# Kernel tuning notes

Measured on AMD Instinct MI355X. Metric: run time of the kernel, lower is better.

The kernel has to match this reference:

```python
import jax, jax.numpy as jnp
import numpy as np

N, IN_F, OUT_F = 8192, 256, 128
ALPHA = 0.2          # LeakyReLU negative slope
NEG_INF = -9e15      # mask value used by the original module
DENSITY = 0.1        # adjacency density


def setup_inputs() -> dict:
    key = jax.random.key(0)
    k1, k2, k3, k4 = jax.random.split(key, 4)
    x = jax.random.normal(k1, (N, IN_F), dtype=jnp.float32)
    adj = (jax.random.uniform(k2, (N, N)) < DENSITY).astype(jnp.float32)
    W = jax.random.normal(k3, (IN_F, OUT_F), dtype=jnp.float32) * (1.0 / np.sqrt(IN_F))
    a = jax.random.normal(k4, (2 * OUT_F, 1), dtype=jnp.float32) * (1.0 / np.sqrt(2 * OUT_F))
    return {"x": x, "adj": adj, "W": W, "a": a}


def reference(x, adj, W, a):
    # h = x @ W : [N, F]
    h = x @ W
    # Decompose a^T [h_i ; h_j] = (h a1)_i + (h a2)_j  -- identical math to the
    # original O(N^2 * 2F) cat/repeat construction, without materializing it.
    a1 = a[:OUT_F, 0]           # [F]
    a2 = a[OUT_F:, 0]           # [F]
    s1 = h @ a1                 # [N]
    s2 = h @ a2                 # [N]
    e = jax.nn.leaky_relu(s1[:, None] + s2[None, :], negative_slope=ALPHA)  # [N, N]
    scores = jnp.where(adj > 0, e, NEG_INF)
    attention = jax.nn.softmax(scores, axis=1)   # row-wise softmax
    # dropout = 0.0 (eval mode) -> identity
    h_prime = attention @ h      # [N, F]
    return h_prime
```

## Files before the change

### kernel.cpp

```cpp
#include <hip/hip_runtime.h>
#include <hip/hip_bf16.h>

typedef __attribute__((ext_vector_type(4))) float  f32x4;
typedef __attribute__((ext_vector_type(8))) short  bf16x8;
typedef unsigned short u16;

#define ALPHA 0.2f
#define NN 8192
#define FF 128
#define LOG2E 1.4426950408889634f

__device__ __forceinline__ u16 f2b(float f) {
  __hip_bfloat16 hb = __float2bfloat16(f);
  return *reinterpret_cast<u16*>(&hb);
}

extern "C" __global__ void __launch_bounds__(256)
wt_cvt(const float* __restrict__ x, const float* __restrict__ Wm,
       u16* __restrict__ xb, u16* __restrict__ WTb) {
  const int id = blockIdx.x * 256 + threadIdx.x;
  if (blockIdx.x < 2048) {
    const f32x4 v = *(const f32x4*)(x + (size_t)id * 4);
    uint2 p;
    p.x = f2b(v.x) | ((unsigned)f2b(v.y) << 16);
    p.y = f2b(v.z) | ((unsigned)f2b(v.w) << 16);
    *(uint2*)(xb + (size_t)id * 4) = p;
  } else {
    const int o = id - 2048 * 256;
    const int c = o >> 8, k = o & 255;
    WTb[o] = f2b(Wm[k * 128 + c]);
  }
}

extern "C" __global__ void __launch_bounds__(256)
gat_h(const u16* __restrict__ xb, const u16* __restrict__ WTb,
      const float* __restrict__ av, u16* __restrict__ hT2,
      float* __restrict__ s1v, float* __restrict__ s2v) {
  __shared__ float hs[16][128];
  const int t = threadIdx.x, lane = t & 63, wv = t >> 6;
  const int i0 = blockIdx.x * 16;
  const int fr = lane & 15, kg = lane >> 4;

  f32x4 acc0 = {0.f,0.f,0.f,0.f}, acc1 = {0.f,0.f,0.f,0.f};
  const u16* xp  = xb  + (size_t)(i0 + fr) * 256 + kg * 8;
  const u16* b0p = WTb + (size_t)(wv * 32 + fr) * 256 + kg * 8;
  const u16* b1p = b0p + 16 * 256;
#pragma unroll
  for (int ks = 0; ks < 8; ++ks) {
    const bf16x8 A  = *(const bf16x8*)(xp  + ks * 32);
    const bf16x8 B0 = *(const bf16x8*)(b0p + ks * 32);
    const bf16x8 B1 = *(const bf16x8*)(b1p + ks * 32);
    acc0 = __builtin_amdgcn_mfma_f32_16x16x32_bf16(A, B0, acc0, 0, 0, 0);
    acc1 = __builtin_amdgcn_mfma_f32_16x16x32_bf16(A, B1, acc1, 0, 0, 0);
  }
#pragma unroll
  for (int r = 0; r < 4; ++r) {
    hs[kg * 4 + r][wv * 32 + fr]      = acc0[r];
    hs[kg * 4 + r][wv * 32 + 16 + fr] = acc1[r];
  }
  __syncthreads();

  {
    const int c = t >> 1, rr = (t & 1) * 8;
    u16 u[8];
#pragma unroll
    for (int m = 0; m < 8; ++m) u[m] = f2b(hs[rr + m][c]);
    *(uint4*)(hT2 + ((size_t)(i0 >> 5) * 128 + c) * 32 + (i0 & 31) + rr) =
        *(const uint4*)u;
  }
  {
    const int r = t >> 4, q = t & 15;
    float p1 = 0.f, p2 = 0.f;
#pragma unroll
    for (int m = 0; m < 8; ++m) {
      const int c = q * 8 + m;
      const float hv = hs[r][c];
      p1 = fmaf(hv, av[c], p1);
      p2 = fmaf(hv, av[128 + c], p2);
    }
    p1 += __shfl_xor(p1, 1); p1 += __shfl_xor(p1, 2);
    p1 += __shfl_xor(p1, 4); p1 += __shfl_xor(p1, 8);
    p2 += __shfl_xor(p2, 1); p2 += __shfl_xor(p2, 2);
    p2 += __shfl_xor(p2, 4); p2 += __shfl_xor(p2, 8);
    if (q == 0) { s1v[i0 + r] = p1 * LOG2E; s2v[i0 + r] = p2 * LOG2E; }
  }
}

#define MM(BB, AA) AA = __builtin_amdgcn_mfma_f32_16x16x32_bf16(af, BB, AA, 0, 0, 0)

extern "C" __global__ void __launch_bounds__(256, 4)
gat_main(const float* __restrict__ adj, const u16* __restrict__ hT2,
         const float* __restrict__ s1l, const float* __restrict__ s2l,
         float* __restrict__ out) {
  __shared__ float accp[4][16][132];
  __shared__ float denp[4][16];

  const int t = threadIdx.x, lane = t & 63, ks = t >> 6;
  const int fr = lane & 15, kg = lane >> 4;
  const int i0 = blockIdx.x * 16;

  const float s1i = s1l[i0 + fr];
  const float* adjp = adj + (size_t)(i0 + fr) * NN + ks * 32 + kg * 8;
  const float* s2p  = s2l + ks * 32 + kg * 8;
  const u16*   hp   = hT2 + ks * 4096 + fr * 32 + kg * 8;

  f32x4 acc0 = {0,0,0,0}, acc1 = {0,0,0,0}, acc2 = {0,0,0,0}, acc3 = {0,0,0,0};
  f32x4 acc4 = {0,0,0,0}, acc5 = {0,0,0,0}, acc6 = {0,0,0,0}, acc7 = {0,0,0,0};
  float den = 0.f;

  f32x4 a0 = *(const f32x4*)(adjp);
  f32x4 a1 = *(const f32x4*)(adjp + 4);
  f32x4 z0 = *(const f32x4*)(s2p);
  f32x4 z1 = *(const f32x4*)(s2p + 4);

  for (int it = 0; it < 64; ++it) {
    const u16* hb = hp + it * 16384;
    const bf16x8 b0 = *(const bf16x8*)(hb);
    const bf16x8 b1 = *(const bf16x8*)(hb + 512);
    const bf16x8 b2 = *(const bf16x8*)(hb + 1024);
    const bf16x8 b3 = *(const bf16x8*)(hb + 1536);
    const bf16x8 b4 = *(const bf16x8*)(hb + 2048);
    const bf16x8 b5 = *(const bf16x8*)(hb + 2560);
    const bf16x8 b6 = *(const bf16x8*)(hb + 3072);
    const bf16x8 b7 = *(const bf16x8*)(hb + 3584);
    __builtin_amdgcn_sched_barrier(0);

    bf16x8 af;
    float dstep = 0.f;
#pragma unroll
    for (int e = 0; e < 8; ++e) {
      const float adv = (e < 4) ? a0[e] : a1[e - 4];
      const float tz  = s1i + ((e < 4) ? z0[e] : z1[e - 4]);
      const float fz  = fmaxf(tz, ALPHA * tz);
      const float w8  = adv * exp2f(fz);
      dstep += w8;
      af[e] = (short)f2b(w8);
    }
    den += dstep;

    const int itn = it < 63 ? it + 1 : 63;
    const float* an = adjp + itn * 128;
    a0 = *(const f32x4*)(an);
    a1 = *(const f32x4*)(an + 4);
    const float* zn = s2p + itn * 128;
    z0 = *(const f32x4*)(zn);
    z1 = *(const f32x4*)(zn + 4);
    __builtin_amdgcn_sched_barrier(0);

    MM(b0, acc0); MM(b1, acc1); MM(b2, acc2); MM(b3, acc3);
    MM(b4, acc4); MM(b5, acc5); MM(b6, acc6); MM(b7, acc7);
  }

  den += __shfl_xor(den, 16);
  den += __shfl_xor(den, 32);
  if (lane < 16) denp[ks][fr] = den;

#define STACC(F, AA) _Pragma("unroll") \
  for (int r = 0; r < 4; ++r) accp[ks][kg * 4 + r][F * 16 + fr] = AA[r];
  STACC(0, acc0) STACC(1, acc1) STACC(2, acc2) STACC(3, acc3)
  STACC(4, acc4) STACC(5, acc5) STACC(6, acc6) STACC(7, acc7)
#undef STACC

  __syncthreads();

  {
    const int row = t >> 4;
    const int c0  = (t & 15) * 8;
    const float dv = denp[0][row] + denp[1][row] + denp[2][row] + denp[3][row];
    f32x4 sA = {0,0,0,0}, sB = {0,0,0,0};
#pragma unroll
    for (int w = 0; w < 4; ++w) {
      sA += *(const f32x4*)&accp[w][row][c0];
      sB += *(const f32x4*)&accp[w][row][c0 + 4];
    }
    const float inv = 1.f / dv;
    sA *= inv; sB *= inv;
    float* op = out + (size_t)(i0 + row) * FF + c0;
    *(f32x4*)op       = sA;
    *(f32x4*)(op + 4) = sB;
  }
}

extern "C" void kernel_launch(void* const* d_in, const int* in_sizes, int n_in,
                              void* d_out, int out_size, void* d_ws, size_t ws_size,
                              hipStream_t stream) {
  const float* x   = (const float*)d_in[0];
  const float* adj = (const float*)d_in[1];
  const float* Wm  = (const float*)d_in[2];
  const float* av  = (const float*)d_in[3];
  float* out = (float*)d_out;

  char* ws = (char*)d_ws;
  u16*   hT2 = (u16*)(ws);
  float* s1v = (float*)(ws + 2097152);
  float* s2v = (float*)(ws + 2129920);
  u16*   xb  = (u16*)(ws + 2162688);
  u16*   WTb = (u16*)(ws + 6356992);

  wt_cvt  <<<2176, 256, 0, stream>>>(x, Wm, xb, WTb);
  gat_h   <<<NN / 16, 256, 0, stream>>>(xb, WTb, av, hT2, s1v, s2v);
  gat_main<<<NN / 16, 256, 0, stream>>>(adj, hT2, s1v, s2v, out);
}
```

Before: 417.8 us.

## Split columns four ways and compute two row tiles per block with reduction

gat_main now handles 32 rows per block instead of 16, so each h fragment loaded from memory feeds two MFMAs. It also splits the 8192 columns into four quarters across blocks and writes partial numerators and denominators to workspace. A new gat_red kernel sums the four partials and normalises. This aims to halve h-tile traffic and lengthen the MFMA chain per load while keeping 1024 blocks. The cost is more accumulator registers, roughly 16 MB of partial writes and reads, and an extra kernel launch.

```diff
diff --git a/kernel.cpp b/kernel.cpp
--- a/kernel.cpp
+++ b/kernel.cpp
@@ -86,99 +86,153 @@
   }
 }
 
-#define MM(BB, AA) AA = __builtin_amdgcn_mfma_f32_16x16x32_bf16(af, BB, AA, 0, 0, 0)
+#define MM(BB, AA) AA = __builtin_amdgcn_mfma_f32_16x16x32_bf16(af0, BB, AA, 0, 0, 0)
+#define MM1(BB, AA) AA = __builtin_amdgcn_mfma_f32_16x16x32_bf16(af1, BB, AA, 0, 0, 0)
 
 extern "C" __global__ void __launch_bounds__(256, 4)
 gat_main(const float* __restrict__ adj, const u16* __restrict__ hT2,
          const float* __restrict__ s1l, const float* __restrict__ s2l,
-         float* __restrict__ out) {
+         float* __restrict__ nump, float* __restrict__ deng) {
   __shared__ float accp[4][16][132];
   __shared__ float denp[4][16];
 
   const int t = threadIdx.x, lane = t & 63, ks = t >> 6;
   const int fr = lane & 15, kg = lane >> 4;
-  const int i0 = blockIdx.x * 16;
-
-  const float s1i = s1l[i0 + fr];
-  const float* adjp = adj + (size_t)(i0 + fr) * NN + ks * 32 + kg * 8;
-  const float* s2p  = s2l + ks * 32 + kg * 8;
-  const u16*   hp   = hT2 + ks * 4096 + fr * 32 + kg * 8;
-
-  f32x4 acc0 = {0,0,0,0}, acc1 = {0,0,0,0}, acc2 = {0,0,0,0}, acc3 = {0,0,0,0};
-  f32x4 acc4 = {0,0,0,0}, acc5 = {0,0,0,0}, acc6 = {0,0,0,0}, acc7 = {0,0,0,0};
-  float den = 0.f;
-
-  f32x4 a0 = *(const f32x4*)(adjp);
-  f32x4 a1 = *(const f32x4*)(adjp + 4);
+  const int tile = blockIdx.x >> 2, q = blockIdx.x & 3;
+  const int i0 = tile * 32;
+  const int jq = q * 2048;
+
+  const float s1i0 = s1l[i0 + fr];
+  const float s1i1 = s1l[i0 + 16 + fr];
+  const float* adjp0 = adj + (size_t)(i0 + fr) * NN + jq + ks * 32 + kg * 8;
+  const float* adjp1 = adjp0 + (size_t)16 * NN;
+  const float* s2p   = s2l + jq + ks * 32 + kg * 8;
+  const u16*   hp    = hT2 + (size_t)(q * 64 + ks) * 4096 + fr * 32 + kg * 8;
+
+  f32x4 acc0[8], acc1[8];
+#pragma unroll
+  for (int f = 0; f < 8; ++f) { acc0[f] = (f32x4){0,0,0,0}; acc1[f] = (f32x4){0,0,0,0}; }
+  float den0 = 0.f, den1 = 0.f;
+
+  f32x4 a0 = *(const f32x4*)(adjp0);
+  f32x4 a1 = *(const f32x4*)(adjp0 + 4);
+  f32x4 a2 = *(const f32x4*)(adjp1);
+  f32x4 a3 = *(const f32x4*)(adjp1 + 4);
   f32x4 z0 = *(const f32x4*)(s2p);
   f32x4 z1 = *(const f32x4*)(s2p + 4);
 
-  for (int it = 0; it < 64; ++it) {
+  for (int it = 0; it < 16; ++it) {
     const u16* hb = hp + it * 16384;
     const bf16x8 b0 = *(const bf16x8*)(hb);
     const bf16x8 b1 = *(const bf16x8*)(hb + 512);
     const bf16x8 b2 = *(const bf16x8*)(hb + 1024);
     const bf16x8 b3 = *(const bf16x8*)(hb + 1536);
+    __builtin_amdgcn_sched_barrier(0);
+
+    bf16x8 af0, af1;
+    float d0 = 0.f, d1 = 0.f;
+#pragma unroll
+    for (int e = 0; e < 8; ++e) {
+      const float zz  = (e < 4) ? z0[e] : z1[e - 4];
+      const float av0 = (e < 4) ? a0[e] : a1[e - 4];
+      const float av1 = (e < 4) ? a2[e] : a3[e - 4];
+      float t0 = s1i0 + zz; t0 = fmaxf(t0, ALPHA * t0);
+      float t1 = s1i1 + zz; t1 = fmaxf(t1, ALPHA * t1);
+      const float w0 = av0 * exp2f(t0);
+      const float w1 = av1 * exp2f(t1);
+      d0 += w0; d1 += w1;
+      af0[e] = (short)f2b(w0);
+      af1[e] = (short)f2b(w1);
+    }
+    den0 += d0; den1 += d1;
+    __builtin_amdgcn_sched_barrier(0);
+
     const bf16x8 b4 = *(const bf16x8*)(hb + 2048);
     const bf16x8 b5 = *(const bf16x8*)(hb + 2560);
     const bf16x8 b6 = *(const bf16x8*)(hb + 3072);
     const bf16x8 b7 = *(const bf16x8*)(hb + 3584);
     __builtin_amdgcn_sched_barrier(0);
 
-    bf16x8 af;
-    float dstep = 0.f;
-#pragma unroll
-    for (int e = 0; e < 8; ++e) {
-      const float adv = (e < 4) ? a0[e] : a1[e - 4];
-      const float tz  = s1i + ((e < 4) ? z0[e] : z1[e - 4]);
-      const float fz  = fmaxf(tz, ALPHA * tz);
-      const float w8  = adv * exp2f(fz);
-      dstep += w8;
-      af[e] = (short)f2b(w8);
-    }
-    den += dstep;
-
-    const int itn = it < 63 ? it + 1 : 63;
-    const float* an = adjp + itn * 128;
-    a0 = *(const f32x4*)(an);
-    a1 = *(const f32x4*)(an + 4);
-    const float* zn = s2p + itn * 128;
-    z0 = *(const f32x4*)(zn);
-    z1 = *(const f32x4*)(zn + 4);
-    __builtin_amdgcn_sched_barrier(0);
-
-    MM(b0, acc0); MM(b1, acc1); MM(b2, acc2); MM(b3, acc3);
-    MM(b4, acc4); MM(b5, acc5); MM(b6, acc6); MM(b7, acc7);
-  }
-
-  den += __shfl_xor(den, 16);
-  den += __shfl_xor(den, 32);
-  if (lane < 16) denp[ks][fr] = den;
-
-#define STACC(F, AA) _Pragma("unroll") \
-  for (int r = 0; r < 4; ++r) accp[ks][kg * 4 + r][F * 16 + fr] = AA[r];
-  STACC(0, acc0) STACC(1, acc1) STACC(2, acc2) STACC(3, acc3)
-  STACC(4, acc4) STACC(5, acc5) STACC(6, acc6) STACC(7, acc7)
-#undef STACC
-
-  __syncthreads();
-
-  {
-    const int row = t >> 4;
-    const int c0  = (t & 15) * 8;
-    const float dv = denp[0][row] + denp[1][row] + denp[2][row] + denp[3][row];
+    MM(b0, acc0[0]); MM1(b0, acc1[0]); MM(b1, acc0[1]); MM1(b1, acc1[1]);
+    MM(b2, acc0[2]); MM1(b2, acc1[2]); MM(b3, acc0[3]); MM1(b3, acc1[3]);
+
+    const int itn = it < 15 ? it + 1 : 15;
+    a0 = *(const f32x4*)(adjp0 + itn * 128);
+    a1 = *(const f32x4*)(adjp0 + itn * 128 + 4);
+    a2 = *(const f32x4*)(adjp1 + itn * 128);
+    a3 = *(const f32x4*)(adjp1 + itn * 128 + 4);
+    z0 = *(const f32x4*)(s2p + itn * 128);
+    z1 = *(const f32x4*)(s2p + itn * 128 + 4);
+    __builtin_amdgcn_sched_barrier(0);
+
+    MM(b4, acc0[4]); MM1(b4, acc1[4]); MM(b5, acc0[5]); MM1(b5, acc1[5]);
+    MM(b6, acc0[6]); MM1(b6, acc1[6]); MM(b7, acc0[7]); MM1(b7, acc1[7]);
+  }
+
+  const size_t obase = ((size_t)(q * 256 + tile)) * 32;
+
+  {
+    float d = den0;
+    d += __shfl_xor(d, 16); d += __shfl_xor(d, 32);
+    if (lane < 16) denp[ks][fr] = d;
+#pragma unroll
+    for (int f = 0; f < 8; ++f)
+#pragma unroll
+      for (int r = 0; r < 4; ++r) accp[ks][kg * 4 + r][f * 16 + fr] = acc0[f][r];
+    __syncthreads();
+    const int row = t >> 4, c0 = (t & 15) * 8;
     f32x4 sA = {0,0,0,0}, sB = {0,0,0,0};
 #pragma unroll
     for (int w = 0; w < 4; ++w) {
       sA += *(const f32x4*)&accp[w][row][c0];
       sB += *(const f32x4*)&accp[w][row][c0 + 4];
     }
-    const float inv = 1.f / dv;
-    sA *= inv; sB *= inv;
-    float* op = out + (size_t)(i0 + row) * FF + c0;
-    *(f32x4*)op       = sA;
-    *(f32x4*)(op + 4) = sB;
-  }
+    float* op = nump + (obase + row) * FF + c0;
+    *(f32x4*)op = sA; *(f32x4*)(op + 4) = sB;
+    if ((t & 15) == 0)
+      deng[obase + row] = denp[0][row] + denp[1][row] + denp[2][row] + denp[3][row];
+    __syncthreads();
+  }
+  {
+    float d = den1;
+    d += __shfl_xor(d, 16); d += __shfl_xor(d, 32);
+    if (lane < 16) denp[ks][fr] = d;
+#pragma unroll
+    for (int f = 0; f < 8; ++f)
+#pragma unroll
+      for (int r = 0; r < 4; ++r) accp[ks][kg * 4 + r][f * 16 + fr] = acc1[f][r];
+    __syncthreads();
+    const int row = t >> 4, c0 = (t & 15) * 8;
+    f32x4 sA = {0,0,0,0}, sB = {0,0,0,0};
+#pragma unroll
+    for (int w = 0; w < 4; ++w) {
+      sA += *(const f32x4*)&accp[w][row][c0];
+      sB += *(const f32x4*)&accp[w][row][c0 + 4];
+    }
+    float* op = nump + (obase + 16 + row) * FF + c0;
+    *(f32x4*)op = sA; *(f32x4*)(op + 4) = sB;
+    if ((t & 15) == 0)
+      deng[obase + 16 + row] = denp[0][row] + denp[1][row] + denp[2][row] + denp[3][row];
+  }
+}
+
+extern "C" __global__ void __launch_bounds__(256)
+gat_red(const float* __restrict__ nump, const float* __restrict__ deng,
+        float* __restrict__ out) {
+  const int gid = blockIdx.x * 256 + threadIdx.x;
+  const int i = gid >> 5, c4 = (gid & 31) * 4;
+  const int tile = i >> 5, row = i & 31;
+  f32x4 s = {0,0,0,0};
+  float dv = 0.f;
+#pragma unroll
+  for (int q = 0; q < 4; ++q) {
+    const size_t rb = ((size_t)(q * 256 + tile)) * 32 + row;
+    s  += *(const f32x4*)(nump + rb * FF + c4);
+    dv += deng[rb];
+  }
+  const float inv = 1.f / dv;
+  s *= inv;
+  *(f32x4*)(out + (size_t)i * FF + c4) = s;
 }
 
 extern "C" void kernel_launch(void* const* d_in, const int* in_sizes, int n_in,
@@ -196,8 +250,11 @@
   float* s2v = (float*)(ws + 2129920);
   u16*   xb  = (u16*)(ws + 2162688);
   u16*   WTb = (u16*)(ws + 6356992);
+  float* nump = (float*)(ws + 6422528);
+  float* deng = (float*)(ws + 23199744);
 
   wt_cvt  <<<2176, 256, 0, stream>>>(x, Wm, xb, WTb);
   gat_h   <<<NN / 16, 256, 0, stream>>>(xb, WTb, av, hT2, s1v, s2v);
-  gat_main<<<NN / 16, 256, 0, stream>>>(adj, hT2, s1v, s2v, out);
-}
+  gat_main<<<1024, 256, 0, stream>>>(adj, hT2, s1v, s2v, nump, deng);
+  gat_red <<<1024, 256, 0, stream>>>(nump, deng, out);
+}
```

After: 454.8 us. +8.8%, slower.
